# Optimization experiments

Hardware: AMD Instinct MI355X
Metric: run time of the kernel (lower is better)

Reference implementation:

```python
import jax, jax.numpy as jnp
import numpy as np

SIGMA = 0.3
EPS = 1e-8  # torch CosineSimilarity eps
_LOG_NORM_CONST = float(np.log(SIGMA) + 0.5 * np.log(2.0 * np.pi))


def _normal_log_prob(x):
    # Normal(loc=1, scale=SIGMA).log_prob(x)
    z = (x - 1.0) / SIGMA
    return -0.5 * z * z - _LOG_NORM_CONST


def setup_inputs() -> dict:
    key = jax.random.key(0)
    kx, ky = jax.random.split(key)
    ex = jax.random.normal(kx, (8192, 1024), dtype=jnp.float32)
    ey = jax.random.normal(ky, (8192, 1024), dtype=jnp.float32)
    return {"ex": ex, "ey": ey}


def reference(ex, ey):
    # Cosine similarity [N, M] via normalized matmul (same math as the
    # broadcasted torch CosineSimilarity, without the N*M*D intermediate).
    exn = ex / jnp.maximum(jnp.linalg.norm(ex, axis=-1, keepdims=True), EPS)
    eyn = ey / jnp.maximum(jnp.linalg.norm(ey, axis=-1, keepdims=True), EPS)
    C = jnp.einsum('nd,md->nm', exn, eyn)
    C1 = _normal_log_prob(jnp.max(C, axis=-1)).sum()  # best match per ex row
    C2 = _normal_log_prob(jnp.max(C, axis=0)).sum()   # best match per ey row
    return (C1, C2)
```

## Files before the change

### kernel.cpp

```cpp
#include <hip/hip_runtime.h>

#define D_DIM 1024
#define NROWS 8192

typedef float f32x4 __attribute__((ext_vector_type(4)));
typedef long  i64x2 __attribute__((ext_vector_type(2)));

typedef const __attribute__((address_space(1))) void* gaddr_t;
typedef __attribute__((address_space(3))) void* laddr_t;

__device__ __forceinline__ void load16_to_lds(const void* g, void* l) {
    __builtin_amdgcn_global_load_lds((gaddr_t)g, (laddr_t)l, 16, 0, 0);
}

__global__ __launch_bounds__(256) void normalize_rows(const float* __restrict__ ex,
                                                      const float* __restrict__ ey,
                                                      unsigned char* __restrict__ Aq,
                                                      unsigned char* __restrict__ Bq,
                                                      int* __restrict__ maxenc) {
    const int wave = threadIdx.x >> 6, lane = threadIdx.x & 63;
    const int r = blockIdx.x * 4 + wave;
    if (lane == 0) maxenc[r] = 0;

    const float* src;
    unsigned char* dst;
    if (r < NROWS) { src = ex + (size_t)r * D_DIM;           dst = Aq + (size_t)r * D_DIM; }
    else           { src = ey + (size_t)(r - NROWS) * D_DIM; dst = Bq + (size_t)(r - NROWS) * D_DIM; }

    float4 v[4];
    float ss = 0.0f;
    #pragma unroll
    for (int j = 0; j < 4; ++j) {
        v[j] = ((const float4*)src)[lane + 64 * j];
        ss += v[j].x * v[j].x + v[j].y * v[j].y + v[j].z * v[j].z + v[j].w * v[j].w;
    }
    #pragma unroll
    for (int off = 32; off; off >>= 1) ss += __shfl_xor(ss, off, 64);
    float scale = 1.0f / fmaxf(sqrtf(ss), 1e-8f);

    #pragma unroll
    for (int j = 0; j < 4; ++j) {
        int p = (lane + 64 * j) << 2;
        int blk = p >> 7, w = p & 127;
        int s = w >> 5, f = (w >> 3) & 3, b = w & 7;
        int q = blk * 128 + (f + ((s >> 1) << 2)) * 16 + (s & 1) * 8 + b;
        int pk = 0;
        pk = __builtin_amdgcn_cvt_pk_fp8_f32(v[j].x * scale, v[j].y * scale, pk, false);
        pk = __builtin_amdgcn_cvt_pk_fp8_f32(v[j].z * scale, v[j].w * scale, pk, true);
        ((int*)dst)[q >> 2] = pk;
    }
}

__global__ __launch_bounds__(256) void gemm_max(const unsigned char* __restrict__ A,
                                                const unsigned char* __restrict__ B,
                                                int* __restrict__ rowmax,
                                                int* __restrict__ colmax) {
    __shared__ __align__(16) unsigned char Alds[128 * 128];
    __shared__ __align__(16) unsigned char Blds[128 * 128];

    const int bm = blockIdx.x >> 6;
    const int bn = blockIdx.x & 63;
    const int rowb = bm * 128;
    const int colb = bn * 128;

    const int t    = threadIdx.x;
    const int lane = t & 63;
    const int wave = t >> 6;
    const int wm = (wave & 1) * 64;
    const int wn = (wave >> 1) * 64;
    const int fr = lane & 15;
    const int fq = lane >> 4;
    const int pos1 = (fq ^ (fr & 7)) * 16;
    const int pos2 = pos1 ^ 64;

    const int srow = t >> 3;
    const int scol = ((t ^ (t >> 3)) & 7) * 16;

    const unsigned char* Ag = A + (size_t)(rowb + srow) * D_DIM + scol;
    const unsigned char* Bg = B + (size_t)(colb + srow) * D_DIM + scol;

    f32x4 acc[4][4] = {};

    for (int kt = 0; kt < D_DIM; kt += 128) {
        #pragma unroll
        for (int i = 0; i < 4; ++i)
            load16_to_lds(Ag + (size_t)i * 32 * D_DIM + kt,
                          (char*)Alds + i * 4096 + wave * 1024);
        #pragma unroll
        for (int i = 0; i < 4; ++i)
            load16_to_lds(Bg + (size_t)i * 32 * D_DIM + kt,
                          (char*)Blds + i * 4096 + wave * 1024);
        __syncthreads();

        i64x2 a1[4], a2[4];
        #pragma unroll
        for (int i = 0; i < 4; ++i) {
            const unsigned char* p = Alds + (wm + i * 16 + fr) * 128;
            a1[i] = *(const i64x2*)(p + pos1);
            a2[i] = *(const i64x2*)(p + pos2);
        }
        #pragma unroll
        for (int j = 0; j < 4; ++j) {
            const unsigned char* p = Blds + (wn + j * 16 + fr) * 128;
            i64x2 b1 = *(const i64x2*)(p + pos1);
            i64x2 b2 = *(const i64x2*)(p + pos2);
            #pragma unroll
            for (int i = 0; i < 4; ++i) {
                acc[i][j] = __builtin_amdgcn_mfma_f32_16x16x32_fp8_fp8(a1[i][0], b1[0], acc[i][j], 0, 0, 0);
                acc[i][j] = __builtin_amdgcn_mfma_f32_16x16x32_fp8_fp8(a1[i][1], b1[1], acc[i][j], 0, 0, 0);
                acc[i][j] = __builtin_amdgcn_mfma_f32_16x16x32_fp8_fp8(a2[i][0], b2[0], acc[i][j], 0, 0, 0);
                acc[i][j] = __builtin_amdgcn_mfma_f32_16x16x32_fp8_fp8(a2[i][1], b2[1], acc[i][j], 0, 0, 0);
            }
        }
        __syncthreads();
    }

    const float SH = 2.0f;

    #pragma unroll
    for (int i = 0; i < 4; ++i) {
        #pragma unroll
        for (int r = 0; r < 4; ++r) {
            float m = fmaxf(fmaxf(acc[i][0][r], acc[i][1][r]),
                            fmaxf(acc[i][2][r], acc[i][3][r]));
            m = fmaxf(m, __shfl_xor(m, 1, 64));
            m = fmaxf(m, __shfl_xor(m, 2, 64));
            m = fmaxf(m, __shfl_xor(m, 4, 64));
            m = fmaxf(m, __shfl_xor(m, 8, 64));
            if (fr == 0) {
                int row = rowb + wm + i * 16 + fq * 4 + r;
                atomicMax(&rowmax[row], __float_as_int(m + SH));
            }
        }
    }
    #pragma unroll
    for (int j = 0; j < 4; ++j) {
        float m = -1e30f;
        #pragma unroll
        for (int i = 0; i < 4; ++i)
            #pragma unroll
            for (int r = 0; r < 4; ++r)
                m = fmaxf(m, acc[i][j][r]);
        m = fmaxf(m, __shfl_xor(m, 16, 64));
        m = fmaxf(m, __shfl_xor(m, 32, 64));
        if (fq == 0) {
            int col = colb + wn + j * 16 + fr;
            atomicMax(&colmax[col], __float_as_int(m + SH));
        }
    }
}

__global__ __launch_bounds__(256) void finalize(const int* __restrict__ rowmax,
                                                const int* __restrict__ colmax,
                                                float* __restrict__ out) {
    const int* src = (blockIdx.x == 0) ? rowmax : colmax;
    int t = threadIdx.x;
    float s = 0.0f;
    for (int i = t; i < NROWS; i += 256) {
        float v = __int_as_float(src[i]) - 2.0f;
        float z = (v - 1.0f) * (1.0f / 0.3f);
        s += -0.5f * z * z + 0.2850342711212634f;
    }
    #pragma unroll
    for (int off = 32; off; off >>= 1) s += __shfl_xor(s, off, 64);
    __shared__ float wsum[4];
    if ((t & 63) == 0) wsum[t >> 6] = s;
    __syncthreads();
    if (t == 0) out[blockIdx.x] = wsum[0] + wsum[1] + wsum[2] + wsum[3];
}

extern "C" void kernel_launch(void* const* d_in, const int* in_sizes, int n_in,
                              void* d_out, int out_size, void* d_ws, size_t ws_size,
                              hipStream_t stream) {
    const float* ex = (const float*)d_in[0];
    const float* ey = (const float*)d_in[1];
    float* out = (float*)d_out;

    char* ws = (char*)d_ws;
    unsigned char* Aq = (unsigned char*)ws;
    unsigned char* Bq = (unsigned char*)(ws + (size_t)NROWS * D_DIM);
    int* rowmax = (int*)(ws + (size_t)2 * NROWS * D_DIM);
    int* colmax = rowmax + NROWS;

    normalize_rows<<<(2 * NROWS) / 4, 256, 0, stream>>>(ex, ey, Aq, Bq, rowmax);
    gemm_max<<<64 * 64, 256, 0, stream>>>(Aq, Bq, rowmax, colmax);
    finalize<<<2, 256, 0, stream>>>(rowmax, colmax, out);
}
```

Before: 207.3 us.

## Double-buffer LDS with 64-wide K tiles to overlap loads with MFMA

```diff
diff --git a/kernel.cpp b/kernel.cpp
--- a/kernel.cpp
+++ b/kernel.cpp
@@ -41,9 +41,9 @@
     #pragma unroll
     for (int j = 0; j < 4; ++j) {
         int p = (lane + 64 * j) << 2;
-        int blk = p >> 7, w = p & 127;
+        int blk = p >> 6, w = p & 63;
         int s = w >> 5, f = (w >> 3) & 3, b = w & 7;
-        int q = blk * 128 + (f + ((s >> 1) << 2)) * 16 + (s & 1) * 8 + b;
+        int q = blk * 64 + f * 16 + s * 8 + b;
         int pk = 0;
         pk = __builtin_amdgcn_cvt_pk_fp8_f32(v[j].x * scale, v[j].y * scale, pk, false);
         pk = __builtin_amdgcn_cvt_pk_fp8_f32(v[j].z * scale, v[j].w * scale, pk, true);
@@ -55,8 +55,7 @@
                                                 const unsigned char* __restrict__ B,
                                                 int* __restrict__ rowmax,
                                                 int* __restrict__ colmax) {
-    __shared__ __align__(16) unsigned char Alds[128 * 128];
-    __shared__ __align__(16) unsigned char Blds[128 * 128];
+    __shared__ __align__(16) unsigned char Lds[2][16384];
 
     const int bm = blockIdx.x >> 6;
     const int bn = blockIdx.x & 63;
@@ -70,46 +69,55 @@
     const int wn = (wave >> 1) * 64;
     const int fr = lane & 15;
     const int fq = lane >> 4;
-    const int pos1 = (fq ^ (fr & 7)) * 16;
-    const int pos2 = pos1 ^ 64;
+    const int fpos = (fq ^ ((fr >> 1) & 3)) * 16;
 
-    const int srow = t >> 3;
-    const int scol = ((t ^ (t >> 3)) & 7) * 16;
+    const int srow1 = wave * 16 + (lane >> 2);
+    const int srow2 = 64 + srow1;
+    const int spos = lane & 3;
+    const int c1 = (spos ^ ((srow1 >> 1) & 3)) * 16;
+    const int c2 = (spos ^ ((srow2 >> 1) & 3)) * 16;
 
-    const unsigned char* Ag = A + (size_t)(rowb + srow) * D_DIM + scol;
-    const unsigned char* Bg = B + (size_t)(colb + srow) * D_DIM + scol;
+    const unsigned char* Ag1 = A + (size_t)(rowb + srow1) * D_DIM + c1;
+    const unsigned char* Ag2 = A + (size_t)(rowb + srow2) * D_DIM + c2;
+    const unsigned char* Bg1 = B + (size_t)(colb + srow1) * D_DIM + c1;
+    const unsigned char* Bg2 = B + (size_t)(colb + srow2) * D_DIM + c2;
 
     f32x4 acc[4][4] = {};
 
-    for (int kt = 0; kt < D_DIM; kt += 128) {
+    {
+        unsigned char* d = &Lds[0][0] + wave * 1024;
+        load16_to_lds(Ag1, d);
+        load16_to_lds(Ag2, d + 4096);
+        load16_to_lds(Bg1, d + 8192);
+        load16_to_lds(Bg2, d + 12288);
+    }
+    __syncthreads();
+
+    #pragma unroll 2
+    for (int kt = 0; kt < 16; ++kt) {
+        if (kt < 15) {
+            const int ko = (kt + 1) * 64;
+            unsigned char* d = &Lds[(kt + 1) & 1][0] + wave * 1024;
+            load16_to_lds(Ag1 + ko, d);
+            load16_to_lds(Ag2 + ko, d + 4096);
+            load16_to_lds(Bg1 + ko, d + 8192);
+            load16_to_lds(Bg2 + ko, d + 12288);
+        }
+
+        const unsigned char* Ab = &Lds[kt & 1][0];
+        const unsigned char* Bb = Ab + 8192;
+
+        i64x2 av[4];
         #pragma unroll
         for (int i = 0; i < 4; ++i)
-            load16_to_lds(Ag + (size_t)i * 32 * D_DIM + kt,
-                          (char*)Alds + i * 4096 + wave * 1024);
-        #pragma unroll
-        for (int i = 0; i < 4; ++i)
-            load16_to_lds(Bg + (size_t)i * 32 * D_DIM + kt,
-                          (char*)Blds + i * 4096 + wave * 1024);
-        __syncthreads();
-
-        i64x2 a1[4], a2[4];
-        #pragma unroll
-        for (int i = 0; i < 4; ++i) {
-            const unsigned char* p = Alds + (wm + i * 16 + fr) * 128;
-            a1[i] = *(const i64x2*)(p + pos1);
-            a2[i] = *(const i64x2*)(p + pos2);
-        }
+            av[i] = *(const i64x2*)(Ab + (wm + i * 16 + fr) * 64 + fpos);
         #pragma unroll
         for (int j = 0; j < 4; ++j) {
-            const unsigned char* p = Blds + (wn + j * 16 + fr) * 128;
-            i64x2 b1 = *(const i64x2*)(p + pos1);
-            i64x2 b2 = *(const i64x2*)(p + pos2);
+            i64x2 bv = *(const i64x2*)(Bb + (wn + j * 16 + fr) * 64 + fpos);
             #pragma unroll
             for (int i = 0; i < 4; ++i) {
-                acc[i][j] = __builtin_amdgcn_mfma_f32_16x16x32_fp8_fp8(a1[i][0], b1[0], acc[i][j], 0, 0, 0);
-                acc[i][j] = __builtin_amdgcn_mfma_f32_16x16x32_fp8_fp8(a1[i][1], b1[1], acc[i][j], 0, 0, 0);
-                acc[i][j] = __builtin_amdgcn_mfma_f32_16x16x32_fp8_fp8(a2[i][0], b2[0], acc[i][j], 0, 0, 0);
-                acc[i][j] = __builtin_amdgcn_mfma_f32_16x16x32_fp8_fp8(a2[i][1], b2[1], acc[i][j], 0, 0, 0);
+                acc[i][j] = __builtin_amdgcn_mfma_f32_16x16x32_fp8_fp8(av[i][0], bv[0], acc[i][j], 0, 0, 0);
+                acc[i][j] = __builtin_amdgcn_mfma_f32_16x16x32_fp8_fp8(av[i][1], bv[1], acc[i][j], 0, 0, 0);
             }
         }
         __syncthreads();
```

New measurement: 220.0 us. 1.06x slower.
